# Kernel optimization log

Measured on AMD Instinct MI355X. Metric: run time of the kernel, lower is better.

## Reference

```python
import jax, jax.numpy as jnp
import numpy as np
from jax import lax

LBDA = 0.1
EPS = 0.01
NUM_CLASSES = 20


def setup_inputs() -> dict:
    key = jax.random.key(0)
    k1, k2 = jax.random.split(key)
    target_features = jax.random.normal(k1, (2048, 8, 2048), dtype=jnp.float32)
    support_features = jax.random.normal(k2, (100, 8, 2048), dtype=jnp.float32)
    # 20-way 5-shot: every class present so per-class mean is well defined
    support_labels = jnp.repeat(jnp.arange(NUM_CLASSES, dtype=jnp.int32), 100 // NUM_CLASSES)
    return {
        "target_features": target_features,
        "support_features": support_features,
        "support_labels": support_labels,
    }


def _softmin(xs, lbda):
    # -lbda * log(sum_i exp(-x_i/lbda)), stable
    return -lbda * jax.nn.logsumexp(jnp.stack([-x / lbda for x in xs], axis=0), axis=0)


def otam_cum_dist(dists, lbda=LBDA):
    # dists: [Q, Sp, L, S] frame distance matrices
    d = jnp.pad(dists, ((0, 0), (0, 0), (0, 0), (1, 1)))  # pad columns -> M = S + 2
    M = d.shape[-1]
    # row 0: running sum along columns (cum[0,0] = d[0,0] = 0 from padding)
    row0 = jnp.cumsum(d[:, :, 0, :], axis=-1)

    def step(prev_row, d_row):
        # prev_row, d_row: [Q, Sp, M]; column 0 is never written -> stays 0
        cur = [jnp.zeros_like(d_row[..., 0])]
        cur.append(d_row[..., 1] + _softmin([prev_row[..., 0], prev_row[..., 1], cur[0]], lbda))
        for m in range(2, M - 1):
            cur.append(d_row[..., m] + _softmin([prev_row[..., m - 1], cur[m - 1]], lbda))
        cur.append(d_row[..., M - 1] + _softmin([prev_row[..., M - 2], prev_row[..., M - 1], cur[M - 2]], lbda))
        new_row = jnp.stack(cur, axis=-1)
        return new_row, None

    d_rows = jnp.moveaxis(d[:, :, 1:, :], 2, 0)  # [L-1, Q, Sp, M]
    final_row, _ = lax.scan(step, row0, d_rows)
    return final_row[..., -1]  # [Q, Sp]


def cos_sim(x, y, eps=EPS):
    num = x @ y.T
    den = jnp.linalg.norm(x, axis=-1)[:, None] * jnp.linalg.norm(y, axis=-1)[None, :] + eps
    return num / den


def reference(target_features, support_features, support_labels):
    Q, S, D = target_features.shape
    Sp = support_features.shape[0]
    tf = target_features.reshape(Q * S, D)
    sf = support_features.reshape(Sp * S, D)
    frame_dists = 1.0 - cos_sim(tf, sf)  # [Q*S, Sp*S]
    # '(tb ts) (sb ss) -> tb sb ts ss'
    dists = frame_dists.reshape(Q, S, Sp, S).transpose(0, 2, 1, 3)
    cum_dists = otam_cum_dist(dists) + otam_cum_dist(dists.transpose(0, 1, 3, 2))  # [Q, Sp]
    # per-class mean over support (torch.unique returns sorted labels 0..C-1)
    onehot = (support_labels[:, None] == jnp.arange(NUM_CLASSES)[None, :]).astype(cum_dists.dtype)
    onehot = onehot / jnp.sum(onehot, axis=0, keepdims=True)
    class_dists = cum_dists @ onehot  # [Q, C]
    return -class_dists[None]  # logits [1, Q, C]
```

## Files before the change

### kernel.cpp

```cpp
#include <hip/hip_runtime.h>

#define QN    2048
#define SS    8
#define DD    2048
#define SP    100
#define NCLS  20
#define MROWS (QN*SS)
#define NROWS (SP*SS)
#define NPAD  832
#define KK    DD

typedef __bf16 bf16x8 __attribute__((ext_vector_type(8)));
typedef float  f32x4  __attribute__((ext_vector_type(4)));

__device__ __forceinline__ unsigned short f2bf(float f) {
    unsigned int u = __float_as_uint(f);
    u += 0x7fffu + ((u >> 16) & 1u);
    return (unsigned short)(u >> 16);
}

__global__ void cvt_kernel(const float* __restrict__ tf, const float* __restrict__ sf,
                           unsigned short* __restrict__ Abf, unsigned short* __restrict__ Bbf,
                           float* __restrict__ nA, float* __restrict__ nB)
{
    const int wv   = threadIdx.x >> 6;
    const int lane = threadIdx.x & 63;
    const int row  = blockIdx.x * 4 + wv;

    const float* src = nullptr;
    unsigned short* dst;
    float* nrm; int r;
    if (row < MROWS) { src = tf + (size_t)row * DD; dst = Abf + (size_t)row * DD; nrm = nA; r = row; }
    else {
        r = row - MROWS;
        dst = Bbf + (size_t)r * DD; nrm = nB;
        if (r < NROWS) src = sf + (size_t)r * DD;
    }

    float s = 0.f;
#pragma unroll
    for (int j = 0; j < 8; j++) {
        ushort4 pk = make_ushort4(0, 0, 0, 0);
        if (src) {
            float4 v = *(const float4*)(src + j * 256 + lane * 4);
            s += v.x*v.x + v.y*v.y + v.z*v.z + v.w*v.w;
            pk = make_ushort4(f2bf(v.x), f2bf(v.y), f2bf(v.z), f2bf(v.w));
        }
        *(ushort4*)(dst + j * 256 + lane * 4) = pk;
    }
#pragma unroll
    for (int o = 32; o; o >>= 1) s += __shfl_down(s, o);
    if (lane == 0) nrm[r] = sqrtf(s);
}

__device__ __forceinline__ float softmin2(float a, float b) {
    float mn = fminf(a, b), mx = fmaxf(a, b);
    return mn - 0.1f * __logf(1.0f + __expf((mn - mx) * 10.0f));
}
__device__ __forceinline__ float softmin3(float a, float b, float c) {
    float mn = fminf(fminf(a, b), c);
    float sum = __expf((mn - a) * 10.0f) + __expf((mn - b) * 10.0f) + __expf((mn - c) * 10.0f);
    return mn - 0.1f * __logf(sum);
}

__device__ __forceinline__ void gld16(const void* g, void* l) {
    __builtin_amdgcn_global_load_lds(
        (const __attribute__((address_space(1))) unsigned int*)g,
        (__attribute__((address_space(3))) unsigned int*)l, 16, 0, 0);
}

__device__ __forceinline__ float cellf(const uint4* raw, int a, int b) {
    const unsigned* p = (const unsigned*)raw;
    unsigned wv = p[a * 4 + (b >> 1)];
    return __uint_as_float((b & 1) ? (wv & 0xffff0000u) : (wv << 16));
}

__device__ __forceinline__ float otam_dp(const uint4* raw, int dir) {
    float prev[10], cur[10];
    prev[0] = 0.f;
#pragma unroll
    for (int m = 1; m <= 8; m++) {
        float v0 = cellf(raw, 0, m - 1), v1 = cellf(raw, m - 1, 0);
        prev[m] = prev[m - 1] + (dir ? v1 : v0);
    }
    prev[9] = prev[8];
#pragma unroll
    for (int l = 1; l < 8; l++) {
        float d[8];
#pragma unroll
        for (int j = 0; j < 8; j++) {
            float v0 = cellf(raw, l, j), v1 = cellf(raw, j, l);
            d[j] = dir ? v1 : v0;
        }
        cur[1] = d[0] + softmin3(prev[0], prev[1], 0.0f);
#pragma unroll
        for (int m = 2; m <= 8; m++)
            cur[m] = d[m - 1] + softmin2(prev[m - 1], cur[m - 1]);
        cur[9] = softmin3(prev[8], prev[9], cur[8]);
#pragma unroll
        for (int m = 1; m < 10; m++) prev[m] = cur[m];
    }
    return prev[9];
}

#define EBS (32 * 72)

__global__ __launch_bounds__(256, 4) void gemm_full(
    const unsigned short* __restrict__ A,
    const unsigned short* __restrict__ B,
    const float* __restrict__ nA, const float* __restrict__ nB,
    const int* __restrict__ labels,
    float* __restrict__ out)
{
    __shared__ __align__(16) unsigned short smem[4 * EBS];
    unsigned short* Als = smem;
    unsigned short* Bls = smem + 4096;

    const int mt  = blockIdx.x;
    const int nt  = blockIdx.y;
    const int tid = threadIdx.x;
    const int lane = tid & 63;
    const int w    = tid >> 6;
    const int wm   = (w & 1) * 64, wn = (w >> 1) * 64;
    const int col  = lane & 15, kg = lane >> 4;

    f32x4 acc[4][4] = {};

    const int c0 = tid, c1 = tid + 256;
    const unsigned short* Ab0 = A + (size_t)(mt * 128 + (c0 >> 2)) * KK + (c0 & 3) * 8;
    const unsigned short* Ab1 = A + (size_t)(mt * 128 + (c1 >> 2)) * KK + (c1 & 3) * 8;
    const unsigned short* Bb0 = B + (size_t)(nt * 128 + (c0 >> 2)) * KK + (c0 & 3) * 8;
    const unsigned short* Bb1 = B + (size_t)(nt * 128 + (c1 >> 2)) * KK + (c1 & 3) * 8;

    for (int kk = 0; kk < KK; kk += 32) {
        __syncthreads();
        gld16(Ab0 + kk, (char*)Als + c0 * 16);
        gld16(Ab1 + kk, (char*)Als + c1 * 16);
        gld16(Bb0 + kk, (char*)Bls + c0 * 16);
        gld16(Bb1 + kk, (char*)Bls + c1 * 16);
        __syncthreads();
        bf16x8 af[4], bfr[4];
#pragma unroll
        for (int i = 0; i < 4; i++) af[i]  = *(const bf16x8*)(Als + (wm + i * 16 + col) * 32 + kg * 8);
#pragma unroll
        for (int i = 0; i < 4; i++) bfr[i] = *(const bf16x8*)(Bls + (wn + i * 16 + col) * 32 + kg * 8);
#pragma unroll
        for (int mi = 0; mi < 4; mi++)
#pragma unroll
            for (int ni = 0; ni < 4; ni++)
                acc[mi][ni] = __builtin_amdgcn_mfma_f32_16x16x32_bf16(af[mi], bfr[ni], acc[mi][ni], 0, 0, 0);
    }

    __syncthreads();

    unsigned short* eb = smem + w * EBS;
    const int mbase = mt * 128 + wm;
    const int nbase = nt * 128 + wn;
    const int pr  = lane & 31;
    const int qv2 = pr >> 3, sv = pr & 7;
    const int dir = lane >> 5;

#pragma unroll
    for (int p = 0; p < 2; p++) {
        if (p) __syncthreads();
#pragma unroll
        for (int mi2 = 0; mi2 < 2; mi2++) {
            const int mi = p * 2 + mi2;
            float nx[4];
#pragma unroll
            for (int r = 0; r < 4; r++) nx[r] = nA[mbase + mi * 16 + kg * 4 + r];
#pragma unroll
            for (int ni = 0; ni < 4; ni++) {
                const float ny = nB[nbase + ni * 16 + col];
#pragma unroll
                for (int r = 0; r < 4; r++) {
                    float d = 1.0f - acc[mi][ni][r] * __builtin_amdgcn_rcpf(nx[r] * ny + 0.01f);
                    eb[(mi2 * 16 + kg * 4 + r) * 72 + ni * 16 + col] = f2bf(d);
                }
            }
        }
        __syncthreads();

        uint4 raw[8];
        const unsigned short* tb = eb + (qv2 * 8) * 72 + sv * 8;
#pragma unroll
        for (int l = 0; l < 8; l++) raw[l] = *(const uint4*)(tb + l * 72);

        float res = otam_dp(raw, dir);
        res += __shfl_down(res, 32);
        if (dir == 0) {
            const int qg = mt * 16 + (wm >> 3) + p * 4 + qv2;
            const int sg = nt * 16 + (wn >> 3) + sv;
            if (sg < SP) atomicAdd(out + (size_t)qg * NCLS + labels[sg], -res * 0.2f);
        }
    }
}

#define EBH (64 * 40)

__global__ __launch_bounds__(256, 4) void gemm_half(
    const unsigned short* __restrict__ A,
    const unsigned short* __restrict__ B,
    const float* __restrict__ nA, const float* __restrict__ nB,
    const int* __restrict__ labels,
    float* __restrict__ out)
{
    __shared__ __align__(16) unsigned short smem[4 * EBH];
    unsigned short* Als = smem;
    unsigned short* Bls = smem + 4096;

    const int mt  = blockIdx.x;
    const int tid = threadIdx.x;
    const int lane = tid & 63;
    const int w    = tid >> 6;
    const int wm   = (w & 1) * 64, wn = (w >> 1) * 32;
    const int col  = lane & 15, kg = lane >> 4;

    f32x4 acc[4][2] = {};

    const int c0 = tid, c1 = tid + 256;
    const unsigned short* Ab0 = A + (size_t)(mt * 128 + (c0 >> 2)) * KK + (c0 & 3) * 8;
    const unsigned short* Ab1 = A + (size_t)(mt * 128 + (c1 >> 2)) * KK + (c1 & 3) * 8;
    const unsigned short* Bb0 = B + (size_t)(768 + (c0 >> 2)) * KK + (c0 & 3) * 8;

    for (int kk = 0; kk < KK; kk += 32) {
        __syncthreads();
        gld16(Ab0 + kk, (char*)Als + c0 * 16);
        gld16(Ab1 + kk, (char*)Als + c1 * 16);
        gld16(Bb0 + kk, (char*)Bls + c0 * 16);
        __syncthreads();
        bf16x8 af[4], bfr[2];
#pragma unroll
        for (int i = 0; i < 4; i++) af[i]  = *(const bf16x8*)(Als + (wm + i * 16 + col) * 32 + kg * 8);
#pragma unroll
        for (int i = 0; i < 2; i++) bfr[i] = *(const bf16x8*)(Bls + (wn + i * 16 + col) * 32 + kg * 8);
#pragma unroll
        for (int mi = 0; mi < 4; mi++)
#pragma unroll
            for (int ni = 0; ni < 2; ni++)
                acc[mi][ni] = __builtin_amdgcn_mfma_f32_16x16x32_bf16(af[mi], bfr[ni], acc[mi][ni], 0, 0, 0);
    }

    __syncthreads();

    unsigned short* eb = smem + w * EBH;
    const int mbase = mt * 128 + wm;
    const int nbase = 768 + wn;

#pragma unroll
    for (int mi = 0; mi < 4; mi++) {
        float nx[4];
#pragma unroll
        for (int r = 0; r < 4; r++) nx[r] = nA[mbase + mi * 16 + kg * 4 + r];
#pragma unroll
        for (int ni = 0; ni < 2; ni++) {
            const float ny = nB[nbase + ni * 16 + col];
#pragma unroll
            for (int r = 0; r < 4; r++) {
                float d = 1.0f - acc[mi][ni][r] * __builtin_amdgcn_rcpf(nx[r] * ny + 0.01f);
                eb[(mi * 16 + kg * 4 + r) * 40 + ni * 16 + col] = f2bf(d);
            }
        }
    }
    __syncthreads();

    const int pr  = lane & 31;
    const int qv  = pr >> 2, sv = pr & 3;
    const int dir = lane >> 5;
    uint4 raw[8];
    const unsigned short* tb = eb + (qv * 8) * 40 + sv * 8;
#pragma unroll
    for (int l = 0; l < 8; l++) raw[l] = *(const uint4*)(tb + l * 40);

    float res = otam_dp(raw, dir);
    res += __shfl_down(res, 32);
    if (dir == 0) {
        const int qg = mt * 16 + (wm >> 3) + qv;
        const int sg = 96 + (wn >> 3) + sv;
        if (sg < SP) atomicAdd(out + (size_t)qg * NCLS + labels[sg], -res * 0.2f);
    }
}

extern "C" void kernel_launch(void* const* d_in, const int* in_sizes, int n_in,
                              void* d_out, int out_size, void* d_ws, size_t ws_size,
                              hipStream_t stream)
{
    const float* tf     = (const float*)d_in[0];
    const float* sf     = (const float*)d_in[1];
    const int*   labels = (const int*)d_in[2];
    float* out = (float*)d_out;

    char* ws = (char*)d_ws;
    const size_t szA    = (size_t)MROWS * KK * 2;
    const size_t szB    = (size_t)NPAD  * KK * 2;
    const size_t szNA   = (size_t)MROWS * 4;
    unsigned short* Abf = (unsigned short*)ws;
    unsigned short* Bbf = (unsigned short*)(ws + szA);
    float* nA   = (float*)(ws + szA + szB);
    float* nB   = (float*)(ws + szA + szB + szNA);

    hipMemsetAsync(out, 0, (size_t)QN * NCLS * sizeof(float), stream);
    cvt_kernel<<<(MROWS + NPAD) / 4, 256, 0, stream>>>(tf, sf, Abf, Bbf, nA, nB);
    gemm_full<<<dim3(MROWS / 128, 6), 256, 0, stream>>>(Abf, Bbf, nA, nB, labels, out);
    gemm_half<<<MROWS / 128, 256, 0, stream>>>(Abf, Bbf, nA, nB, labels, out);
}
```

Measured before the change: 315.2 us.

## Merge gemm kernels into one launch, fold output zeroing into convert kernel

Zeroes the output inside the conversion kernel, replacing the separate memset. The two GEMM+DP kernels become one launch, with a seventh grid column handling the tail 32 padded support rows as a narrower 128x32 tile. B padding shrinks from 832 to 800 rows, so less zero-filled data is converted and loaded. The launch-bounds occupancy hint drops from 4 to 2, and the fused kernel's shared buffer is sized for the larger path, which may lower occupancy for the tail blocks.

```diff
diff --git a/kernel.cpp b/kernel.cpp
--- a/kernel.cpp
+++ b/kernel.cpp
@@ -7,7 +7,7 @@
 #define NCLS  20
 #define MROWS (QN*SS)
 #define NROWS (SP*SS)
-#define NPAD  832
+#define NPAD  800
 #define KK    DD
 
 typedef __bf16 bf16x8 __attribute__((ext_vector_type(8)));
@@ -21,31 +21,30 @@
 
 __global__ void cvt_kernel(const float* __restrict__ tf, const float* __restrict__ sf,
                            unsigned short* __restrict__ Abf, unsigned short* __restrict__ Bbf,
-                           float* __restrict__ nA, float* __restrict__ nB)
+                           float* __restrict__ nA, float* __restrict__ nB,
+                           float* __restrict__ out)
 {
+    if (blockIdx.x < 160) out[blockIdx.x * 256 + threadIdx.x] = 0.f;
+
     const int wv   = threadIdx.x >> 6;
     const int lane = threadIdx.x & 63;
     const int row  = blockIdx.x * 4 + wv;
 
-    const float* src = nullptr;
+    const float* src;
     unsigned short* dst;
     float* nrm; int r;
     if (row < MROWS) { src = tf + (size_t)row * DD; dst = Abf + (size_t)row * DD; nrm = nA; r = row; }
     else {
         r = row - MROWS;
-        dst = Bbf + (size_t)r * DD; nrm = nB;
-        if (r < NROWS) src = sf + (size_t)r * DD;
+        src = sf + (size_t)r * DD; dst = Bbf + (size_t)r * DD; nrm = nB;
     }
 
     float s = 0.f;
 #pragma unroll
     for (int j = 0; j < 8; j++) {
-        ushort4 pk = make_ushort4(0, 0, 0, 0);
-        if (src) {
-            float4 v = *(const float4*)(src + j * 256 + lane * 4);
-            s += v.x*v.x + v.y*v.y + v.z*v.z + v.w*v.w;
-            pk = make_ushort4(f2bf(v.x), f2bf(v.y), f2bf(v.z), f2bf(v.w));
-        }
+        float4 v = *(const float4*)(src + j * 256 + lane * 4);
+        s += v.x*v.x + v.y*v.y + v.z*v.z + v.w*v.w;
+        ushort4 pk = make_ushort4(f2bf(v.x), f2bf(v.y), f2bf(v.z), f2bf(v.w));
         *(ushort4*)(dst + j * 256 + lane * 4) = pk;
     }
 #pragma unroll
@@ -105,7 +104,7 @@
 
 #define EBS (32 * 72)
 
-__global__ __launch_bounds__(256, 4) void gemm_full(
+__global__ __launch_bounds__(256, 2) void gemm_kernel(
     const unsigned short* __restrict__ A,
     const unsigned short* __restrict__ B,
     const float* __restrict__ nA, const float* __restrict__ nB,
@@ -121,163 +120,139 @@
     const int tid = threadIdx.x;
     const int lane = tid & 63;
     const int w    = tid >> 6;
-    const int wm   = (w & 1) * 64, wn = (w >> 1) * 64;
     const int col  = lane & 15, kg = lane >> 4;
-
-    f32x4 acc[4][4] = {};
+    const int mbase0 = mt * 128;
 
     const int c0 = tid, c1 = tid + 256;
-    const unsigned short* Ab0 = A + (size_t)(mt * 128 + (c0 >> 2)) * KK + (c0 & 3) * 8;
-    const unsigned short* Ab1 = A + (size_t)(mt * 128 + (c1 >> 2)) * KK + (c1 & 3) * 8;
-    const unsigned short* Bb0 = B + (size_t)(nt * 128 + (c0 >> 2)) * KK + (c0 & 3) * 8;
-    const unsigned short* Bb1 = B + (size_t)(nt * 128 + (c1 >> 2)) * KK + (c1 & 3) * 8;
-
-    for (int kk = 0; kk < KK; kk += 32) {
+    const unsigned short* Ab0 = A + (size_t)(mbase0 + (c0 >> 2)) * KK + (c0 & 3) * 8;
+    const unsigned short* Ab1 = A + (size_t)(mbase0 + (c1 >> 2)) * KK + (c1 & 3) * 8;
+
+    if (nt < 6) {
+        const int wm = (w & 1) * 64, wn = (w >> 1) * 64;
+        f32x4 acc[4][4] = {};
+        const unsigned short* Bb0 = B + (size_t)(nt * 128 + (c0 >> 2)) * KK + (c0 & 3) * 8;
+        const unsigned short* Bb1 = B + (size_t)(nt * 128 + (c1 >> 2)) * KK + (c1 & 3) * 8;
+
+        for (int kk = 0; kk < KK; kk += 32) {
+            __syncthreads();
+            gld16(Ab0 + kk, (char*)Als + c0 * 16);
+            gld16(Ab1 + kk, (char*)Als + c1 * 16);
+            gld16(Bb0 + kk, (char*)Bls + c0 * 16);
+            gld16(Bb1 + kk, (char*)Bls + c1 * 16);
+            __syncthreads();
+            bf16x8 af[4], bfr[4];
+#pragma unroll
+            for (int i = 0; i < 4; i++) af[i]  = *(const bf16x8*)(Als + (wm + i * 16 + col) * 32 + kg * 8);
+#pragma unroll
+            for (int i = 0; i < 4; i++) bfr[i] = *(const bf16x8*)(Bls + (wn + i * 16 + col) * 32 + kg * 8);
+#pragma unroll
+            for (int mi = 0; mi < 4; mi++)
+#pragma unroll
+                for (int ni = 0; ni < 4; ni++)
+                    acc[mi][ni] = __builtin_amdgcn_mfma_f32_16x16x32_bf16(af[mi], bfr[ni], acc[mi][ni], 0, 0, 0);
+        }
+
         __syncthreads();
-        gld16(Ab0 + kk, (char*)Als + c0 * 16);
-        gld16(Ab1 + kk, (char*)Als + c1 * 16);
-        gld16(Bb0 + kk, (char*)Bls + c0 * 16);
-        gld16(Bb1 + kk, (char*)Bls + c1 * 16);
+        unsigned short* eb = smem + w * EBS;
+        const int mbase = mbase0 + wm;
+        const int nbase = nt * 128 + wn;
+        const int pr  = lane & 31;
+        const int qv2 = pr >> 3, sv = pr & 7;
+        const int dir = lane >> 5;
+
+#pragma unroll
+        for (int p = 0; p < 2; p++) {
+            if (p) __syncthreads();
+#pragma unroll
+            for (int mi2 = 0; mi2 < 2; mi2++) {
+                const int mi = p * 2 + mi2;
+                float nx[4];
+#pragma unroll
+                for (int r = 0; r < 4; r++) nx[r] = nA[mbase + mi * 16 + kg * 4 + r];
+#pragma unroll
+                for (int ni = 0; ni < 4; ni++) {
+                    const float ny = nB[nbase + ni * 16 + col];
+#pragma unroll
+                    for (int r = 0; r < 4; r++) {
+                        float d = 1.0f - acc[mi][ni][r] * __builtin_amdgcn_rcpf(nx[r] * ny + 0.01f);
+                        eb[(mi2 * 16 + kg * 4 + r) * 72 + ni * 16 + col] = f2bf(d);
+                    }
+                }
+            }
+            __syncthreads();
+
+            uint4 raw[8];
+            const unsigned short* tb = eb + (qv2 * 8) * 72 + sv * 8;
+#pragma unroll
+            for (int l = 0; l < 8; l++) raw[l] = *(const uint4*)(tb + l * 72);
+
+            float res = otam_dp(raw, dir);
+            res += __shfl_down(res, 32);
+            if (dir == 0) {
+                const int qg = mt * 16 + (wm >> 3) + p * 4 + qv2;
+                const int sg = nt * 16 + (wn >> 3) + sv;
+                atomicAdd(out + (size_t)qg * NCLS + labels[sg], -res * 0.2f);
+            }
+        }
+    } else {
+        const int wm = w * 32;
+        f32x4 acc[2][2] = {};
+        const unsigned short* Bb0 = B + (size_t)(768 + (tid >> 2)) * KK + (tid & 3) * 8;
+
+        for (int kk = 0; kk < KK; kk += 32) {
+            __syncthreads();
+            gld16(Ab0 + kk, (char*)Als + c0 * 16);
+            gld16(Ab1 + kk, (char*)Als + c1 * 16);
+            if (tid < 128) gld16(Bb0 + kk, (char*)Bls + tid * 16);
+            __syncthreads();
+            bf16x8 af[2], bfr[2];
+#pragma unroll
+            for (int i = 0; i < 2; i++) af[i]  = *(const bf16x8*)(Als + (wm + i * 16 + col) * 32 + kg * 8);
+#pragma unroll
+            for (int i = 0; i < 2; i++) bfr[i] = *(const bf16x8*)(Bls + (i * 16 + col) * 32 + kg * 8);
+#pragma unroll
+            for (int mi = 0; mi < 2; mi++)
+#pragma unroll
+                for (int ni = 0; ni < 2; ni++)
+                    acc[mi][ni] = __builtin_amdgcn_mfma_f32_16x16x32_bf16(af[mi], bfr[ni], acc[mi][ni], 0, 0, 0);
+        }
+
         __syncthreads();
-        bf16x8 af[4], bfr[4];
-#pragma unroll
-        for (int i = 0; i < 4; i++) af[i]  = *(const bf16x8*)(Als + (wm + i * 16 + col) * 32 + kg * 8);
-#pragma unroll
-        for (int i = 0; i < 4; i++) bfr[i] = *(const bf16x8*)(Bls + (wn + i * 16 + col) * 32 + kg * 8);
-#pragma unroll
-        for (int mi = 0; mi < 4; mi++)
-#pragma unroll
-            for (int ni = 0; ni < 4; ni++)
-                acc[mi][ni] = __builtin_amdgcn_mfma_f32_16x16x32_bf16(af[mi], bfr[ni], acc[mi][ni], 0, 0, 0);
-    }
-
-    __syncthreads();
-
-    unsigned short* eb = smem + w * EBS;
-    const int mbase = mt * 128 + wm;
-    const int nbase = nt * 128 + wn;
-    const int pr  = lane & 31;
-    const int qv2 = pr >> 3, sv = pr & 7;
-    const int dir = lane >> 5;
-
-#pragma unroll
-    for (int p = 0; p < 2; p++) {
-        if (p) __syncthreads();
-#pragma unroll
-        for (int mi2 = 0; mi2 < 2; mi2++) {
-            const int mi = p * 2 + mi2;
+        unsigned short* eb = smem + w * EBS;
+        const int mbase = mbase0 + wm;
+
+#pragma unroll
+        for (int mi = 0; mi < 2; mi++) {
             float nx[4];
 #pragma unroll
             for (int r = 0; r < 4; r++) nx[r] = nA[mbase + mi * 16 + kg * 4 + r];
 #pragma unroll
-            for (int ni = 0; ni < 4; ni++) {
-                const float ny = nB[nbase + ni * 16 + col];
+            for (int ni = 0; ni < 2; ni++) {
+                const float ny = nB[768 + ni * 16 + col];
 #pragma unroll
                 for (int r = 0; r < 4; r++) {
                     float d = 1.0f - acc[mi][ni][r] * __builtin_amdgcn_rcpf(nx[r] * ny + 0.01f);
-                    eb[(mi2 * 16 + kg * 4 + r) * 72 + ni * 16 + col] = f2bf(d);
+                    eb[(mi * 16 + kg * 4 + r) * 40 + ni * 16 + col] = f2bf(d);
                 }
             }
         }
         __syncthreads();
 
+        const int pr  = lane & 31;
+        const int qv2 = (pr & 15) >> 2, sv = pr & 3;
+        const int dir = lane >> 5;
         uint4 raw[8];
-        const unsigned short* tb = eb + (qv2 * 8) * 72 + sv * 8;
-#pragma unroll
-        for (int l = 0; l < 8; l++) raw[l] = *(const uint4*)(tb + l * 72);
+        const unsigned short* tb = eb + (qv2 * 8) * 40 + sv * 8;
+#pragma unroll
+        for (int l = 0; l < 8; l++) raw[l] = *(const uint4*)(tb + l * 40);
 
         float res = otam_dp(raw, dir);
         res += __shfl_down(res, 32);
-        if (dir == 0) {
-            const int qg = mt * 16 + (wm >> 3) + p * 4 + qv2;
-            const int sg = nt * 16 + (wn >> 3) + sv;
-            if (sg < SP) atomicAdd(out + (size_t)qg * NCLS + labels[sg], -res * 0.2f);
-        }
-    }
-}
-
-#define EBH (64 * 40)
-
-__global__ __launch_bounds__(256, 4) void gemm_half(
-    const unsigned short* __restrict__ A,
-    const unsigned short* __restrict__ B,
-    const float* __restrict__ nA, const float* __restrict__ nB,
-    const int* __restrict__ labels,
-    float* __restrict__ out)
-{
-    __shared__ __align__(16) unsigned short smem[4 * EBH];
-    unsigned short* Als = smem;
-    unsigned short* Bls = smem + 4096;
-
-    const int mt  = blockIdx.x;
-    const int tid = threadIdx.x;
-    const int lane = tid & 63;
-    const int w    = tid >> 6;
-    const int wm   = (w & 1) * 64, wn = (w >> 1) * 32;
-    const int col  = lane & 15, kg = lane >> 4;
-
-    f32x4 acc[4][2] = {};
-
-    const int c0 = tid, c1 = tid + 256;
-    const unsigned short* Ab0 = A + (size_t)(mt * 128 + (c0 >> 2)) * KK + (c0 & 3) * 8;
-    const unsigned short* Ab1 = A + (size_t)(mt * 128 + (c1 >> 2)) * KK + (c1 & 3) * 8;
-    const unsigned short* Bb0 = B + (size_t)(768 + (c0 >> 2)) * KK + (c0 & 3) * 8;
-
-    for (int kk = 0; kk < KK; kk += 32) {
-        __syncthreads();
-        gld16(Ab0 + kk, (char*)Als + c0 * 16);
-        gld16(Ab1 + kk, (char*)Als + c1 * 16);
-        gld16(Bb0 + kk, (char*)Bls + c0 * 16);
-        __syncthreads();
-        bf16x8 af[4], bfr[2];
-#pragma unroll
-        for (int i = 0; i < 4; i++) af[i]  = *(const bf16x8*)(Als + (wm + i * 16 + col) * 32 + kg * 8);
-#pragma unroll
-        for (int i = 0; i < 2; i++) bfr[i] = *(const bf16x8*)(Bls + (wn + i * 16 + col) * 32 + kg * 8);
-#pragma unroll
-        for (int mi = 0; mi < 4; mi++)
-#pragma unroll
-            for (int ni = 0; ni < 2; ni++)
-                acc[mi][ni] = __builtin_amdgcn_mfma_f32_16x16x32_bf16(af[mi], bfr[ni], acc[mi][ni], 0, 0, 0);
-    }
-
-    __syncthreads();
-
-    unsigned short* eb = smem + w * EBH;
-    const int mbase = mt * 128 + wm;
-    const int nbase = 768 + wn;
-
-#pragma unroll
-    for (int mi = 0; mi < 4; mi++) {
-        float nx[4];
-#pragma unroll
-        for (int r = 0; r < 4; r++) nx[r] = nA[mbase + mi * 16 + kg * 4 + r];
-#pragma unroll
-        for (int ni = 0; ni < 2; ni++) {
-            const float ny = nB[nbase + ni * 16 + col];
-#pragma unroll
-            for (int r = 0; r < 4; r++) {
-                float d = 1.0f - acc[mi][ni][r] * __builtin_amdgcn_rcpf(nx[r] * ny + 0.01f);
-                eb[(mi * 16 + kg * 4 + r) * 40 + ni * 16 + col] = f2bf(d);
-            }
-        }
-    }
-    __syncthreads();
-
-    const int pr  = lane & 31;
-    const int qv  = pr >> 2, sv = pr & 3;
-    const int dir = lane >> 5;
-    uint4 raw[8];
-    const unsigned short* tb = eb + (qv * 8) * 40 + sv * 8;
-#pragma unroll
-    for (int l = 0; l < 8; l++) raw[l] = *(const uint4*)(tb + l * 40);
-
-    float res = otam_dp(raw, dir);
-    res += __shfl_down(res, 32);
-    if (dir == 0) {
-        const int qg = mt * 16 + (wm >> 3) + qv;
-        const int sg = 96 + (wn >> 3) + sv;
-        if (sg < SP) atomicAdd(out + (size_t)qg * NCLS + labels[sg], -res * 0.2f);
+        if (dir == 0 && pr < 16) {
+            const int qg = mt * 16 + w * 4 + qv2;
+            const int sg = 96 + sv;
+            atomicAdd(out + (size_t)qg * NCLS + labels[sg], -res * 0.2f);
+        }
     }
 }
 
@@ -299,8 +274,6 @@
     float* nA   = (float*)(ws + szA + szB);
     float* nB   = (float*)(ws + szA + szB + szNA);
 
-    hipMemsetAsync(out, 0, (size_t)QN * NCLS * sizeof(float), stream);
-    cvt_kernel<<<(MROWS + NPAD) / 4, 256, 0, stream>>>(tf, sf, Abf, Bbf, nA, nB);
-    gemm_full<<<dim3(MROWS / 128, 6), 256, 0, stream>>>(Abf, Bbf, nA, nB, labels, out);
-    gemm_half<<<MROWS / 128, 256, 0, stream>>>(Abf, Bbf, nA, nB, labels, out);
-}
+    cvt_kernel<<<(MROWS + NPAD) / 4, 256, 0, stream>>>(tf, sf, Abf, Bbf, nA, nB, out);
+    gemm_kernel<<<dim3(MROWS / 128, 7), 256, 0, stream>>>(Abf, Bbf, nA, nB, labels, out);
+}
```

Result: faster. 278.7 us (-11.6%).
